# Performance work log

Hardware: AMD Instinct MI355X
Metric: run time of the kernel (lower is better)

Reference implementation:

```python
import jax, jax.numpy as jnp
import numpy as np

N_NODES = 100000
N_EDGES = 1600000
IN_FEAT = 64
OUT_FEAT = 64


def setup_inputs() -> dict:
    key = jax.random.key(0)
    k_feat, k_src, k_dst, k_tw, k_tb, k_pw, k_pb = jax.random.split(key, 7)
    bound = 1.0 / np.sqrt(IN_FEAT)
    return {
        "feat": jax.random.normal(k_feat, (N_NODES, IN_FEAT), dtype=jnp.float32),
        "src": jax.random.randint(k_src, (N_EDGES,), 0, N_NODES, dtype=jnp.int32),
        "dst": jax.random.randint(k_dst, (N_EDGES,), 0, N_NODES, dtype=jnp.int32),
        "theta_w": jax.random.uniform(k_tw, (OUT_FEAT, IN_FEAT), jnp.float32, -bound, bound),
        "theta_b": jax.random.uniform(k_tb, (OUT_FEAT,), jnp.float32, -bound, bound),
        "phi_w": jax.random.uniform(k_pw, (OUT_FEAT, IN_FEAT), jnp.float32, -bound, bound),
        "phi_b": jax.random.uniform(k_pb, (OUT_FEAT,), jnp.float32, -bound, bound),
    }


def reference(feat, src, dst, theta_w, theta_b, phi_w, phi_b):
    # Two dense projections: h_theta = theta(feat), h_phi = phi(feat)
    h_theta = feat @ theta_w.T + theta_b          # [N, out_feat]
    h_phi = feat @ phi_w.T + phi_b                # [N, out_feat]
    diff = h_phi - h_theta                        # dstdata['x']
    # u_add_v: per-edge message e = h_theta[src] + (h_phi - h_theta)[dst]
    e = h_theta[src] + diff[dst]                  # [E, out_feat]
    # fn.max('e', 'x'): segment max over destination nodes
    out = jax.ops.segment_max(e, dst, num_segments=N_NODES)  # [N, out_feat]
    # DGL fills zero-in-degree destinations with 0 (segment_max yields -inf)
    return jnp.where(jnp.isfinite(out), out, jnp.float32(0))
```

## Files before the change

kernel.cpp:

```cpp
#include <hip/hip_runtime.h>
#include <hip/hip_bf16.h>
#include <hip/hip_fp16.h>

#define F 64
#define BSH 7
#define NBMAX 1024
#define CHUNK 4096
#define EPT 8
#define BCAP 4096
#define WPAD 72

typedef __bf16 bf16x8 __attribute__((ext_vector_type(8)));
typedef float  f32x4  __attribute__((ext_vector_type(4)));
typedef unsigned int uint4v __attribute__((ext_vector_type(4)));

__device__ inline unsigned pkmax(unsigned a, unsigned b) {
    unsigned d;
    asm volatile("v_pk_max_f16 %0, %1, %2" : "=v"(d) : "v"(a), "v"(b));
    return d;
}
__device__ inline uint4v pkmax4(uint4v a, uint4v b) {
    uint4v r;
    r.x = pkmax(a.x, b.x); r.y = pkmax(a.y, b.y);
    r.z = pkmax(a.z, b.z); r.w = pkmax(a.w, b.w);
    return r;
}
__device__ inline float half_lo(unsigned u) {
    union { unsigned short s; _Float16 h; } c; c.s = (unsigned short)(u & 0xFFFF);
    return (float)c.h;
}
__device__ inline float half_hi(unsigned u) {
    union { unsigned short s; _Float16 h; } c; c.s = (unsigned short)(u >> 16);
    return (float)c.h;
}
__device__ inline void casmax(unsigned* a, unsigned val) {
    unsigned old = *a;
    while (true) {
        unsigned nw = pkmax(old, val);
        if (nw == old) break;
        unsigned prev = atomicCAS(a, old, nw);
        if (prev == old) break;
        old = prev;
    }
}

union FusedSh {
    struct { __bf16 w2t[128 * WPAD]; float bias[128]; } p;
    struct { int cur[NBMAX]; int gb[NBMAX]; } b;
};

__global__ __launch_bounds__(512) void fused_proj_bin(
    const float* __restrict__ feat,
    const float* __restrict__ theta_w, const float* __restrict__ theta_b,
    const float* __restrict__ phi_w,  const float* __restrict__ phi_b,
    _Float16* __restrict__ h16, _Float16* __restrict__ d16,
    const int* __restrict__ src, const int* __restrict__ dst,
    int* __restrict__ bcnt, unsigned* __restrict__ packed,
    int n_nodes, int n_edges, int nb, int bin_blocks, int proj_blocks)
{
    __shared__ FusedSh sh;
    const int t = threadIdx.x;

    if (blockIdx.x < bin_blocks) {
        const int base = blockIdx.x * CHUNK;
        const int cnt = min(CHUNK, n_edges - base);

        for (int i = t; i < nb; i += 512) sh.b.cur[i] = 0;
        __syncthreads();

        unsigned w[EPT];
        int      bk[EPT];
        int      rk[EPT];
        const int k0 = t * EPT;

        if (k0 + EPT <= cnt) {
            #pragma unroll
            for (int j = 0; j < EPT; ++j) {
                int k = k0 + j;
                int s = src[base + k], d = dst[base + k];
                w[j]  = ((unsigned)(d & ((1 << BSH) - 1)) << 17) | (unsigned)s;
                int b = d >> BSH;
                bk[j] = b;
                rk[j] = atomicAdd(&sh.b.cur[b], 1);
            }
        } else {
            #pragma unroll
            for (int j = 0; j < EPT; ++j) {
                int k = k0 + j;
                bk[j] = -1;
                if (k < cnt) {
                    int s = src[base + k], d = dst[base + k];
                    w[j]  = ((unsigned)(d & ((1 << BSH) - 1)) << 17) | (unsigned)s;
                    int b = d >> BSH;
                    bk[j] = b;
                    rk[j] = atomicAdd(&sh.b.cur[b], 1);
                }
            }
        }
        __syncthreads();

        for (int i = t; i < nb; i += 512) {
            int c = sh.b.cur[i];
            sh.b.gb[i] = c ? atomicAdd(&bcnt[i], c) : 0;
        }
        __syncthreads();

        #pragma unroll
        for (int j = 0; j < EPT; ++j) {
            if (bk[j] >= 0) {
                int pos = sh.b.gb[bk[j]] + rk[j];
                if (pos < BCAP) packed[(size_t)bk[j] * BCAP + pos] = w[j];
            }
        }
    } else {
        const int pb = blockIdx.x - bin_blocks;

        for (int i = t; i < 128 * 64; i += 512) {
            int n = i >> 6, k = i & 63;
            float v = (n < 64) ? theta_w[n * 64 + k]
                               : phi_w[(n - 64) * 64 + k] - theta_w[(n - 64) * 64 + k];
            sh.p.w2t[n * WPAD + k] = (__bf16)v;
        }
        if (t < 128) {
            int n = t;
            sh.p.bias[n] = (n < 64) ? theta_b[n] : (phi_b[n - 64] - theta_b[n - 64]);
        }
        __syncthreads();

        const int lane = t & 63;
        const int wv   = t >> 6;
        const int m    = lane & 15;
        const int q    = lane >> 4;
        const int nchunks = (n_nodes + 127) >> 7;

        for (int ch = pb; ch < nchunks; ch += proj_blocks) {
            const int rowbase = ch * 128 + wv * 16;
            int arow = rowbase + m;
            int rs = arow < n_nodes ? arow : 0;

            bf16x8 a0, a1;
            {
                const float* p0 = feat + (size_t)rs * 64 + q * 8;
                #pragma unroll
                for (int j = 0; j < 8; ++j) a0[j] = (__bf16)p0[j];
                #pragma unroll
                for (int j = 0; j < 8; ++j) a1[j] = (__bf16)p0[32 + j];
            }

            f32x4 acc[8];
            #pragma unroll
            for (int c = 0; c < 8; ++c) acc[c] = (f32x4){0.f, 0.f, 0.f, 0.f};

            #pragma unroll
            for (int c = 0; c < 8; ++c) {
                const __bf16* wp = &sh.p.w2t[(c * 16 + m) * WPAD + q * 8];
                bf16x8 b0 = *(const bf16x8*)wp;
                bf16x8 b1 = *(const bf16x8*)(wp + 32);
                acc[c] = __builtin_amdgcn_mfma_f32_16x16x32_bf16(a0, b0, acc[c], 0, 0, 0);
                acc[c] = __builtin_amdgcn_mfma_f32_16x16x32_bf16(a1, b1, acc[c], 0, 0, 0);
            }

            #pragma unroll
            for (int c = 0; c < 8; ++c) {
                float bb = sh.p.bias[c * 16 + m];
                #pragma unroll
                for (int r = 0; r < 4; ++r) {
                    int orow = rowbase + q * 4 + r;
                    if (orow < n_nodes) {
                        float v = acc[c][r] + bb;
                        if (c < 4)
                            h16[(size_t)orow * F + c * 16 + m] = (_Float16)v;
                        else
                            d16[(size_t)orow * F + (c - 4) * 16 + m] = (_Float16)v;
                    }
                }
            }
        }
    }
}

__global__ __launch_bounds__(256) void sort_reduce(
    const unsigned* __restrict__ packed, const int* __restrict__ bcnt,
    const _Float16* __restrict__ h16, const _Float16* __restrict__ d16,
    float* __restrict__ out, int n_nodes)
{
    __shared__ unsigned ew[BCAP];
    __shared__ unsigned mx[128 * 32];
    __shared__ int fcnt[128];
    __shared__ int fbg[129];
    __shared__ int fs[256];

    const int b = blockIdx.x, t = threadIdx.x;
    const int beg = b * BCAP;
    const int cnt = min(bcnt[b], BCAP);
    const unsigned NEGI = 0xFC00FC00u;

    #pragma unroll
    for (int i = 0; i < 16; ++i) mx[i * 256 + t] = NEGI;
    if (t < 128) fcnt[t] = 0;
    __syncthreads();

    unsigned w[16];
    int      rk[16];
    #pragma unroll
    for (int j = 0; j < 16; ++j) {
        int k = j * 256 + t;
        rk[j] = -1;
        if (k < cnt) {
            unsigned wrd = packed[beg + k];
            w[j]  = wrd;
            rk[j] = atomicAdd(&fcnt[wrd >> 17], 1);
        }
    }
    __syncthreads();

    int v = (t < 128) ? fcnt[t] : 0;
    fs[t] = v;
    __syncthreads();
    for (int off = 1; off < 128; off <<= 1) {
        int x = (t >= off) ? fs[t - off] : 0;
        __syncthreads();
        fs[t] += x;
        __syncthreads();
    }
    if (t < 128) fbg[t] = fs[t] - v;
    if (t == 0)  fbg[128] = cnt;
    __syncthreads();

    #pragma unroll
    for (int j = 0; j < 16; ++j) {
        if (rk[j] >= 0) {
            unsigned wrd = w[j];
            ew[fbg[wrd >> 17] + rk[j]] = wrd & 0x1FFFFu;
        }
    }
    __syncthreads();

    const int g  = t >> 3;
    const int f8 = t & 7;
    {
        int L0 = (cnt + 31) >> 5;
        int L  = ((L0 + 3) & ~7) | 4;
        int s  = g * L; if (s > cnt) s = cnt;
        int e  = s + L; if (e > cnt) e = cnt;

        if (s < e) {
            int lo = 0, hi = 128;
            while (lo + 1 < hi) {
                int mid = (lo + hi) >> 1;
                if (fbg[mid] <= s) lo = mid; else hi = mid;
            }
            int node = lo;
            int nend = fbg[node + 1];

            uint4v acc = (uint4v){NEGI, NEGI, NEGI, NEGI};
            int p = s;
            for (; p + 4 <= e; p += 4) {
                uint4v sv = *(const uint4v*)&ew[p];
                uint4v v0 = *(const uint4v*)(h16 + (size_t)sv.x * F + f8 * 8);
                uint4v v1 = *(const uint4v*)(h16 + (size_t)sv.y * F + f8 * 8);
                uint4v v2 = *(const uint4v*)(h16 + (size_t)sv.z * F + f8 * 8);
                uint4v v3 = *(const uint4v*)(h16 + (size_t)sv.w * F + f8 * 8);
                while (p >= nend) {
                    unsigned* m0 = &mx[node * 32 + f8 * 4];
                    casmax(m0 + 0, acc.x); casmax(m0 + 1, acc.y);
                    casmax(m0 + 2, acc.z); casmax(m0 + 3, acc.w);
                    acc = (uint4v){NEGI, NEGI, NEGI, NEGI};
                    ++node; nend = fbg[node + 1];
                }
                acc = pkmax4(acc, v0);
                while (p + 1 >= nend) {
                    unsigned* m0 = &mx[node * 32 + f8 * 4];
                    casmax(m0 + 0, acc.x); casmax(m0 + 1, acc.y);
                    casmax(m0 + 2, acc.z); casmax(m0 + 3, acc.w);
                    acc = (uint4v){NEGI, NEGI, NEGI, NEGI};
                    ++node; nend = fbg[node + 1];
                }
                acc = pkmax4(acc, v1);
                while (p + 2 >= nend) {
                    unsigned* m0 = &mx[node * 32 + f8 * 4];
                    casmax(m0 + 0, acc.x); casmax(m0 + 1, acc.y);
                    casmax(m0 + 2, acc.z); casmax(m0 + 3, acc.w);
                    acc = (uint4v){NEGI, NEGI, NEGI, NEGI};
                    ++node; nend = fbg[node + 1];
                }
                acc = pkmax4(acc, v2);
                while (p + 3 >= nend) {
                    unsigned* m0 = &mx[node * 32 + f8 * 4];
                    casmax(m0 + 0, acc.x); casmax(m0 + 1, acc.y);
                    casmax(m0 + 2, acc.z); casmax(m0 + 3, acc.w);
                    acc = (uint4v){NEGI, NEGI, NEGI, NEGI};
                    ++node; nend = fbg[node + 1];
                }
                acc = pkmax4(acc, v3);
            }
            for (; p < e; ++p) {
                unsigned srcn = ew[p];
                uint4v v0 = *(const uint4v*)(h16 + (size_t)srcn * F + f8 * 8);
                while (p >= nend) {
                    unsigned* m0 = &mx[node * 32 + f8 * 4];
                    casmax(m0 + 0, acc.x); casmax(m0 + 1, acc.y);
                    casmax(m0 + 2, acc.z); casmax(m0 + 3, acc.w);
                    acc = (uint4v){NEGI, NEGI, NEGI, NEGI};
                    ++node; nend = fbg[node + 1];
                }
                acc = pkmax4(acc, v0);
            }
            unsigned* m0 = &mx[node * 32 + f8 * 4];
            casmax(m0 + 0, acc.x); casmax(m0 + 1, acc.y);
            casmax(m0 + 2, acc.z); casmax(m0 + 3, acc.w);
        }
    }
    __syncthreads();

    const int ln0 = t >> 3;
    #pragma unroll
    for (int pass = 0; pass < 4; ++pass) {
        int ln = ln0 + pass * 32;
        int node = (b << BSH) + ln;
        if (node < n_nodes) {
            size_t o = (size_t)node * F + f8 * 8;
            f32x4 r0, r1;
            if (fcnt[ln] > 0) {
                uint4v A  = *(const uint4v*)&mx[ln * 32 + f8 * 4];
                uint4v dv = __builtin_nontemporal_load((const uint4v*)(d16 + o));
                r0[0] = half_lo(dv.x) + half_lo(A.x);
                r0[1] = half_hi(dv.x) + half_hi(A.x);
                r0[2] = half_lo(dv.y) + half_lo(A.y);
                r0[3] = half_hi(dv.y) + half_hi(A.y);
                r1[0] = half_lo(dv.z) + half_lo(A.z);
                r1[1] = half_hi(dv.z) + half_hi(A.z);
                r1[2] = half_lo(dv.w) + half_lo(A.w);
                r1[3] = half_hi(dv.w) + half_hi(A.w);
            } else {
                r0 = (f32x4){0.f, 0.f, 0.f, 0.f};
                r1 = (f32x4){0.f, 0.f, 0.f, 0.f};
            }
            __builtin_nontemporal_store(r0, (f32x4*)(out + o));
            __builtin_nontemporal_store(r1, (f32x4*)(out + o + 4));
        }
    }
}

extern "C" void kernel_launch(void* const* d_in, const int* in_sizes, int n_in,
                              void* d_out, int out_size, void* d_ws, size_t ws_size,
                              hipStream_t stream) {
    const float* feat    = (const float*)d_in[0];
    const int*   src     = (const int*)d_in[1];
    const int*   dst     = (const int*)d_in[2];
    const float* theta_w = (const float*)d_in[3];
    const float* theta_b = (const float*)d_in[4];
    const float* phi_w   = (const float*)d_in[5];
    const float* phi_b   = (const float*)d_in[6];
    float* out = (float*)d_out;

    const int n_nodes = in_sizes[0] / F;
    const int n_edges = in_sizes[1];
    const int nb      = (n_nodes + (1 << BSH) - 1) >> BSH;

    _Float16* h16    = (_Float16*)d_ws;
    _Float16* d16    = h16 + (size_t)n_nodes * F;
    unsigned* packed = (unsigned*)(d16 + (size_t)n_nodes * F);
    int*      bcnt   = (int*)(packed + (size_t)nb * BCAP);

    hipMemsetAsync(bcnt, 0, NBMAX * sizeof(int), stream);

    const int bin_blocks  = (n_edges + CHUNK - 1) / CHUNK;
    const int proj_blocks = 391;
    fused_proj_bin<<<bin_blocks + proj_blocks, 512, 0, stream>>>(
        feat, theta_w, theta_b, phi_w, phi_b, h16, d16,
        src, dst, bcnt, packed, n_nodes, n_edges, nb, bin_blocks, proj_blocks);

    sort_reduce<<<nb, 256, 0, stream>>>(packed, bcnt, h16, d16, out, n_nodes);
}
```

Measured before the change: 151.5 us.

## Stage binned edges in LDS sorted by bucket before coalesced global scatter

The binning blocks now compute an exclusive prefix sum of the per-bucket counts in shared memory. They write each packed edge into LDS ordered by bucket, then write to the global packed buffer with consecutive threads handling consecutive sorted slots. Edges landing in the same bucket then go to contiguous global addresses instead of scattered ones. The cost is a shared-memory scan with many barriers, about 24KB more LDS (which may reduce occupancy), and an extra LDS pass. The scan assumes NBMAX is 1024, i.e. two buckets per thread.

```diff
diff --git a/kernel.cpp b/kernel.cpp
--- a/kernel.cpp
+++ b/kernel.cpp
@@ -46,7 +46,12 @@
 
 union FusedSh {
     struct { __bf16 w2t[128 * WPAD]; float bias[128]; } p;
-    struct { int cur[NBMAX]; int gb[NBMAX]; } b;
+    struct {
+        int cur[NBMAX]; int gb[NBMAX]; int lbeg[NBMAX];
+        int fs[512];
+        unsigned sw[CHUNK];
+        unsigned short sb[CHUNK];
+    } b;
 };
 
 __global__ __launch_bounds__(512) void fused_proj_bin(
@@ -65,7 +70,7 @@
         const int base = blockIdx.x * CHUNK;
         const int cnt = min(CHUNK, n_edges - base);
 
-        for (int i = t; i < nb; i += 512) sh.b.cur[i] = 0;
+        for (int i = t; i < NBMAX; i += 512) sh.b.cur[i] = 0;
         __syncthreads();
 
         unsigned w[EPT];
@@ -103,13 +108,42 @@
             int c = sh.b.cur[i];
             sh.b.gb[i] = c ? atomicAdd(&bcnt[i], c) : 0;
         }
+
+        int c0 = sh.b.cur[2 * t];
+        int c1 = sh.b.cur[2 * t + 1];
+        int s2 = c0 + c1;
+        sh.b.fs[t] = s2;
+        __syncthreads();
+        for (int off = 1; off < 512; off <<= 1) {
+            int x = (t >= off) ? sh.b.fs[t - off] : 0;
+            __syncthreads();
+            sh.b.fs[t] += x;
+            __syncthreads();
+        }
+        {
+            int exc = sh.b.fs[t] - s2;
+            sh.b.lbeg[2 * t]     = exc;
+            sh.b.lbeg[2 * t + 1] = exc + c0;
+        }
         __syncthreads();
 
         #pragma unroll
         for (int j = 0; j < EPT; ++j) {
             if (bk[j] >= 0) {
-                int pos = sh.b.gb[bk[j]] + rk[j];
-                if (pos < BCAP) packed[(size_t)bk[j] * BCAP + pos] = w[j];
+                int slot = sh.b.lbeg[bk[j]] + rk[j];
+                sh.b.sw[slot] = w[j];
+                sh.b.sb[slot] = (unsigned short)bk[j];
+            }
+        }
+        __syncthreads();
+
+        #pragma unroll
+        for (int r = 0; r < EPT; ++r) {
+            int p = r * 512 + t;
+            if (p < cnt) {
+                int b = sh.b.sb[p];
+                int pos = sh.b.gb[b] + (p - sh.b.lbeg[b]);
+                if (pos < BCAP) packed[(size_t)b * BCAP + pos] = sh.b.sw[p];
             }
         }
     } else {
```

After: 150.0 us. About the same (-1.0%).
